# Kernel optimization log

Hardware: AMD Instinct MI355X
Metric: run time of the kernel (lower is better)

Reference implementation:

```python
import jax, jax.numpy as jnp
import numpy as np

# Norse LIFParameters defaults (method='super', alpha=100)
DT = 1e-3
TAU_SYN_INV = 200.0   # 1 / 5e-3
TAU_MEM_INV = 100.0   # 1 / 1e-2
V_TH = 1.0
V_LEAK = 0.0
V_RESET = 0.0
ALPHA = 100.0

@jax.custom_vjp
def superspike(x):
    return (x > 0).astype(x.dtype)

def _ss_fwd(x):
    return superspike(x), x

def _ss_bwd(x, g):
    return (g / (ALPHA * jnp.abs(x) + 1.0) ** 2,)

superspike.defvjp(_ss_fwd, _ss_bwd)

T, B, F, H1, OUT = 100, 512, 784, 1024, 10

def setup_inputs() -> dict:
    key = jax.random.key(0)
    k1, k2, k3 = jax.random.split(key, 3)
    x = jax.random.normal(k1, (T, B, F), jnp.float32)
    # fc0: Linear(784, h1) with bias
    W0 = jax.random.normal(k2, (H1, F), jnp.float32) / np.sqrt(F)
    b0 = jnp.zeros((H1,), jnp.float32)
    # LILinearCell input_weights: Linear(h1, 10) without bias
    Wout = jax.random.normal(k3, (OUT, H1), jnp.float32) / np.sqrt(H1)
    return {"x": x, "W0": W0, "b0": b0, "Wout": Wout}

def reference(x, W0, b0, Wout):
    Tn, Bn, Fn = x.shape
    H = W0.shape[0]
    O = Wout.shape[0]

    def step(state, xt):
        v_lif, i_lif, v_li, i_li = state
        z_in = xt @ W0.T + b0                                    # [B, H]
        # LIF cell step
        v_dec = v_lif + DT * TAU_MEM_INV * ((V_LEAK - v_lif) + i_lif)
        i_dec = i_lif * (1.0 - DT * TAU_SYN_INV)
        z = superspike(v_dec - V_TH)                             # spikes [B, H]
        v_new = (1.0 - z) * v_dec + z * V_RESET
        i_new = i_dec + z_in
        # LI linear cell step (voltage output)
        v_li_new = v_li + DT * TAU_MEM_INV * ((V_LEAK - v_li) + i_li)
        i_li_new = i_li * (1.0 - DT * TAU_SYN_INV) + z @ Wout.T  # [B, O]
        return (v_new, i_new, v_li_new, i_li_new), v_li_new

    z0 = lambda s: jnp.zeros(s, x.dtype)
    init = (z0((Bn, H)), z0((Bn, H)), z0((Bn, O)), z0((Bn, O)))
    _, voltages = jax.lax.scan(step, init, x)
    return voltages  # [T, B, 10]
```

## Files before the change

### kernel.cpp

```cpp
#include <hip/hip_runtime.h>

#define T_TOT 100
#define BATCH 512
#define FIN   784
#define HID   1024
#define NOUT  10
#define KP    800
#define BK    32
#define KSTEPS 25

typedef _Float16 f16x8 __attribute__((ext_vector_type(8)));
typedef float    f32x4 __attribute__((ext_vector_type(4)));

#define AS1C(p) ((const __attribute__((address_space(1))) void*)(p))
#define AS3(p)  ((__attribute__((address_space(3))) void*)(p))

__global__ __launch_bounds__(256)
void cvt_split(const float* __restrict__ src, _Float16* __restrict__ hi,
               _Float16* __restrict__ lo, int nrows)
{
    int idx = blockIdx.x * 256 + threadIdx.x;
    if (idx >= nrows * 100) return;
    int row = idx / 100;
    int k0  = (idx - row * 100) * 8;
    f16x8 h, l;
    if (k0 < FIN) {
        float4 a = *(const float4*)(src + (size_t)row * FIN + k0);
        float4 b = *(const float4*)(src + (size_t)row * FIN + k0 + 4);
        float xs[8] = {a.x, a.y, a.z, a.w, b.x, b.y, b.z, b.w};
        #pragma unroll
        for (int j = 0; j < 8; ++j) {
            _Float16 hh = (_Float16)xs[j];
            h[j] = hh;
            l[j] = (_Float16)((xs[j] - (float)hh) * 4096.0f);
        }
    } else {
        #pragma unroll
        for (int j = 0; j < 8; ++j) { h[j] = (_Float16)0.f; l[j] = (_Float16)0.f; }
    }
    *(f16x8*)(hi + (size_t)row * KP + k0) = h;
    *(f16x8*)(lo + (size_t)row * KP + k0) = l;
}

__global__ __launch_bounds__(256, 2)
void gemm_mfma(const _Float16* __restrict__ Xhi, const _Float16* __restrict__ Xlo,
               const _Float16* __restrict__ Whi, const _Float16* __restrict__ Wlo,
               const float* __restrict__ bias, float* __restrict__ Z, int mb)
{
    __shared__ char smem[65536];
    const int tid  = threadIdx.x;
    const int lane = tid & 63;
    const int wid  = tid >> 6;
    const int wm   = wid >> 1;
    const int wn   = wid & 1;
    const int fr   = lane & 15;
    const int fg   = lane >> 4;

    const int j = blockIdx.x;
    int bm, bn;
    if ((mb & 7) == 0) {
        bm = (j & 7) | ((j >> 6) << 3);
        bn = (j >> 3) & 7;
    } else {
        bm = j >> 3;
        bn = j & 7;
    }
    const size_t row0 = (size_t)bm * 128;
    const int    col0 = bn * 128;

    f32x4 accm[4][4], accc[4][4];
    #pragma unroll
    for (int a = 0; a < 4; ++a)
        #pragma unroll
        for (int b = 0; b < 4; ++b) {
            accm[a][b] = (f32x4){0.f, 0.f, 0.f, 0.f};
            accc[a][b] = (f32x4){0.f, 0.f, 0.f, 0.f};
        }

    auto stage = [&](int buf, int kt) {
        const int kof = kt * BK;
        #pragma unroll
        for (int q = 0; q < 2; ++q) {
            const int lin = q * 256 + tid;
            const int row = lin >> 2;
            const int pos = lin & 3;
            const int gg  = pos ^ ((row >> 1) & 3);
            const int ldsw = buf * 32768 + q * 4096 + wid * 1024;
            const size_t ga = (row0 + row) * (size_t)KP + kof + gg * 8;
            const size_t gb = (size_t)(col0 + row) * KP + kof + gg * 8;
            __builtin_amdgcn_global_load_lds(AS1C(Xhi + ga), AS3(smem + ldsw),         16, 0, 0);
            __builtin_amdgcn_global_load_lds(AS1C(Xlo + ga), AS3(smem + ldsw +  8192), 16, 0, 0);
            __builtin_amdgcn_global_load_lds(AS1C(Whi + gb), AS3(smem + ldsw + 16384), 16, 0, 0);
            __builtin_amdgcn_global_load_lds(AS1C(Wlo + gb), AS3(smem + ldsw + 24576), 16, 0, 0);
        }
    };

    auto compute = [&](int buf) {
        const char* base = smem + buf * 32768;
        f16x8 ah[4], al[4], bh[4], bl[4];
        #pragma unroll
        for (int mf = 0; mf < 4; ++mf) {
            const int row = wm * 64 + mf * 16 + fr;
            const int off = row * 64 + ((fg ^ ((row >> 1) & 3)) << 4);
            ah[mf] = *(const f16x8*)(base + off);
            al[mf] = *(const f16x8*)(base + 8192 + off);
        }
        #pragma unroll
        for (int nf = 0; nf < 4; ++nf) {
            const int row = wn * 64 + nf * 16 + fr;
            const int off = row * 64 + ((fg ^ ((row >> 1) & 3)) << 4);
            bh[nf] = *(const f16x8*)(base + 16384 + off);
            bl[nf] = *(const f16x8*)(base + 24576 + off);
        }
        #pragma unroll
        for (int mf = 0; mf < 4; ++mf)
            #pragma unroll
            for (int nf = 0; nf < 4; ++nf) {
                accm[mf][nf] = __builtin_amdgcn_mfma_f32_16x16x32_f16(ah[mf], bh[nf], accm[mf][nf], 0, 0, 0);
                accc[mf][nf] = __builtin_amdgcn_mfma_f32_16x16x32_f16(ah[mf], bl[nf], accc[mf][nf], 0, 0, 0);
                accc[mf][nf] = __builtin_amdgcn_mfma_f32_16x16x32_f16(al[mf], bh[nf], accc[mf][nf], 0, 0, 0);
            }
    };

    stage(0, 0);
    int buf = 0;
    for (int kt = 0; kt < KSTEPS; ++kt) {
        __syncthreads();
        if (kt + 1 < KSTEPS) stage(buf ^ 1, kt + 1);
        compute(buf);
        buf ^= 1;
    }

    #pragma unroll
    for (int nf = 0; nf < 4; ++nf) {
        const int colg = col0 + wn * 64 + nf * 16 + fr;
        const float bv = bias[colg];
        #pragma unroll
        for (int mf = 0; mf < 4; ++mf) {
            const size_t rowg = row0 + wm * 64 + mf * 16 + fg * 4;
            #pragma unroll
            for (int i = 0; i < 4; ++i)
                Z[(rowg + i) * HID + colg] =
                    accm[mf][nf][i] + accc[mf][nf][i] * 2.44140625e-4f + bv;
        }
    }
}

__global__ __launch_bounds__(256, 2)
void lif_scan(const float* __restrict__ Z, const float* __restrict__ Wout,
              float* __restrict__ out,
              float* __restrict__ st_v, float* __restrict__ st_i,
              float* __restrict__ st_vli, float* __restrict__ st_ili,
              int t0, int tn, int first, int last)
{
#pragma clang fp contract(off)
    __shared__ float Wlds[NOUT][HID];
    __shared__ float red[2][4][NOUT];

    const int tid  = threadIdx.x;
    const int b    = blockIdx.x;
    const int h4   = tid * 4;
    const int lane = tid & 63;
    const int wv   = tid >> 6;

    #pragma unroll
    for (int o = 0; o < NOUT; ++o)
        *(float4*)&Wlds[o][h4] = *(const float4*)&Wout[o * HID + h4];

    float v[4], cu[4];
    if (first) {
        #pragma unroll
        for (int j = 0; j < 4; ++j) { v[j] = 0.f; cu[j] = 0.f; }
    } else {
        float4 tv = *(const float4*)&st_v[(size_t)b*HID + h4];
        float4 ti = *(const float4*)&st_i[(size_t)b*HID + h4];
        v[0]=tv.x; v[1]=tv.y; v[2]=tv.z; v[3]=tv.w;
        cu[0]=ti.x; cu[1]=ti.y; cu[2]=ti.z; cu[3]=ti.w;
    }
    float vli = 0.f, ili = 0.f;
    if (!first && tid < NOUT) {
        vli = st_vli[b*NOUT + tid];
        ili = st_ili[b*NOUT + tid];
    }

    __syncthreads();

    const float* Zb = Z + (size_t)b * HID + h4;
    float4 zn = *(const float4*)Zb;

    for (int t = 0; t < tn; ++t) {
        float4 zc = zn;
        if (t + 1 < tn) zn = *(const float4*)(Zb + (size_t)(t+1) * BATCH * HID);

        const float za[4] = {zc.x, zc.y, zc.z, zc.w};
        float zf[4];
        bool anyz = false;
        #pragma unroll
        for (int j = 0; j < 4; ++j) {
            float tmp  = (0.0f - v[j]) + cu[j];
            float vdec = v[j] + 0.1f * tmp;
            bool  z    = vdec > 1.0f;
            zf[j] = z ? 1.0f : 0.0f;
            anyz  = anyz || z;
            v[j]  = z ? 0.0f : vdec;
            cu[j] = cu[j] * 0.8f + za[j];
        }

        float p[NOUT];
        #pragma unroll
        for (int o = 0; o < NOUT; ++o) p[o] = 0.f;

        if (__any(anyz)) {
            if (anyz) {
                #pragma unroll
                for (int o = 0; o < NOUT; ++o) {
                    float4 w = *(const float4*)&Wlds[o][h4];
                    p[o] = zf[0]*w.x + zf[1]*w.y + zf[2]*w.z + zf[3]*w.w;
                }
            }
            #pragma unroll
            for (int o = 0; o < NOUT; ++o) {
                float s = p[o];
                s += __shfl_xor(s, 1);
                s += __shfl_xor(s, 2);
                s += __shfl_xor(s, 4);
                s += __shfl_xor(s, 8);
                s += __shfl_xor(s, 16);
                s += __shfl_xor(s, 32);
                p[o] = s;
            }
        }

        const int par = t & 1;
        if (lane == 0) {
            #pragma unroll
            for (int o = 0; o < NOUT; ++o) red[par][wv][o] = p[o];
        }
        __syncthreads();
        if (tid < NOUT) {
            float s = red[par][0][tid] + red[par][1][tid]
                    + red[par][2][tid] + red[par][3][tid];
            float tmp  = (0.0f - vli) + ili;
            float vnew = vli + 0.1f * tmp;
            ili = ili * 0.8f + s;
            vli = vnew;
            out[((size_t)(t0 + t) * BATCH + b) * NOUT + tid] = vnew;
        }
    }

    if (!last) {
        *(float4*)&st_v[(size_t)b*HID + h4] = make_float4(v[0], v[1], v[2], v[3]);
        *(float4*)&st_i[(size_t)b*HID + h4] = make_float4(cu[0], cu[1], cu[2], cu[3]);
        if (tid < NOUT) { st_vli[b*NOUT + tid] = vli; st_ili[b*NOUT + tid] = ili; }
    }
}

extern "C" void kernel_launch(void* const* d_in, const int* in_sizes, int n_in,
                              void* d_out, int out_size, void* d_ws, size_t ws_size,
                              hipStream_t stream)
{
    const float* x    = (const float*)d_in[0];
    const float* W0   = (const float*)d_in[1];
    const float* b0   = (const float*)d_in[2];
    const float* Wout = (const float*)d_in[3];
    float* out = (float*)d_out;

    char* ws = (char*)d_ws;
    float* st_v   = (float*)ws;
    float* st_i   = st_v   + (size_t)BATCH * HID;
    float* st_vli = st_i   + (size_t)BATCH * HID;
    float* st_ili = st_vli + BATCH * NOUT;
    _Float16* Whi = (_Float16*)(st_ili + BATCH * NOUT);
    _Float16* Wlo = Whi + (size_t)HID * KP;
    char* dyn = (char*)(Wlo + (size_t)HID * KP);

    const size_t fixed = (size_t)(dyn - ws);
    const size_t per_t = (size_t)BATCH * HID * 4
                       + (size_t)BATCH * KP * 2 * 2;
    size_t avail = (ws_size > fixed) ? ws_size - fixed : 0;
    int tch = (int)(avail / per_t);
    if (tch > T_TOT) tch = T_TOT;
    if (tch >= 2) tch &= ~1;
    if (tch < 1) tch = 1;

    float*    Zbuf = (float*)dyn;
    _Float16* Xhi  = (_Float16*)(dyn + (size_t)tch * BATCH * HID * 4);
    _Float16* Xlo  = Xhi + (size_t)tch * BATCH * KP;

    hipLaunchKernelGGL(cvt_split, dim3((HID * 100 + 255) / 256), dim3(256), 0, stream,
                       W0, Whi, Wlo, HID);

    for (int t0 = 0; t0 < T_TOT; t0 += tch) {
        const int tn    = (T_TOT - t0 < tch) ? (T_TOT - t0) : tch;
        const int nrows = tn * BATCH;
        const int mb    = nrows / 128;

        hipLaunchKernelGGL(cvt_split, dim3((nrows * 100 + 255) / 256), dim3(256), 0, stream,
                           x + (size_t)t0 * BATCH * FIN, Xhi, Xlo, nrows);
        hipLaunchKernelGGL(gemm_mfma, dim3(mb * 8), dim3(256), 0, stream,
                           Xhi, Xlo, Whi, Wlo, b0, Zbuf, mb);
        hipLaunchKernelGGL(lif_scan, dim3(BATCH), dim3(256), 0, stream,
                           Zbuf, Wout, out, st_v, st_i, st_vli, st_ili,
                           t0, tn, (t0 == 0) ? 1 : 0, (t0 + tn >= T_TOT) ? 1 : 0);
    }
}
```

Baseline: 537.4 us.

## Use 8-wave GEMM with triple-buffered LDS pipeline and DPP reductions in scan

The GEMM goes from 4 waves to 8 waves per 128x128 tile, with each wave holding half as many accumulators. Staging moves to a 3-stage LDS ring that waits with vmcnt and a raw s_barrier, and MFMA priority is raised with setprio. The block index mapping is also changed for L2 locality. In the LIF scan, the cross-lane reduction becomes DPP sums within 16-lane groups over 16 partial slots, and Z is prefetched two timesteps ahead. Risks: more LDS per block (96KB), which may limit occupancy, and the vmcnt-only wait across waves relies on the barrier for correctness.

```diff
diff --git a/kernel.cpp b/kernel.cpp
--- a/kernel.cpp
+++ b/kernel.cpp
@@ -8,6 +8,14 @@
 #define KP    800
 #define BK    32
 #define KSTEPS 25
+
+#define BM 128
+#define BN 128
+#define BUFSZ 32768
+#define A_HI 0
+#define A_LO 8192
+#define B_HI 16384
+#define B_LO 24576
 
 typedef _Float16 f16x8 __attribute__((ext_vector_type(8)));
 typedef float    f32x4 __attribute__((ext_vector_type(4)));
@@ -42,12 +50,12 @@
     *(f16x8*)(lo + (size_t)row * KP + k0) = l;
 }
 
-__global__ __launch_bounds__(256, 2)
+__global__ __launch_bounds__(512, 2)
 void gemm_mfma(const _Float16* __restrict__ Xhi, const _Float16* __restrict__ Xlo,
                const _Float16* __restrict__ Whi, const _Float16* __restrict__ Wlo,
                const float* __restrict__ bias, float* __restrict__ Z, int mb)
 {
-    __shared__ char smem[65536];
+    __shared__ char smem[3 * BUFSZ];
     const int tid  = threadIdx.x;
     const int lane = tid & 63;
     const int wid  = tid >> 6;
@@ -59,76 +67,80 @@
     const int j = blockIdx.x;
     int bm, bn;
     if ((mb & 7) == 0) {
-        bm = (j & 7) | ((j >> 6) << 3);
-        bn = (j >> 3) & 7;
+        const int x = j & 7, r = j >> 3;
+        bm = x * (mb >> 3) + (r >> 3);
+        bn = r & 7;
     } else {
         bm = j >> 3;
         bn = j & 7;
     }
-    const size_t row0 = (size_t)bm * 128;
-    const int    col0 = bn * 128;
-
-    f32x4 accm[4][4], accc[4][4];
+    const size_t row0 = (size_t)bm * BM;
+    const int    col0 = bn * BN;
+
+    const int srow = tid >> 2;
+    const int spos = tid & 3;
+    const int sgg  = spos ^ ((srow >> 1) & 3);
+    const size_t gax = (row0 + srow) * (size_t)KP + sgg * 8;
+    const size_t gbx = (size_t)(col0 + srow) * KP + sgg * 8;
+    const int ldsw = wid * 1024;
+
+    auto stage = [&](int buf, int kt) {
+        const int kof = kt * BK;
+        const char* dummy;
+        char* base = smem + buf * BUFSZ + ldsw;
+        __builtin_amdgcn_global_load_lds(AS1C(Xhi + gax + kof), AS3(base + A_HI), 16, 0, 0);
+        __builtin_amdgcn_global_load_lds(AS1C(Xlo + gax + kof), AS3(base + A_LO), 16, 0, 0);
+        __builtin_amdgcn_global_load_lds(AS1C(Whi + gbx + kof), AS3(base + B_HI), 16, 0, 0);
+        __builtin_amdgcn_global_load_lds(AS1C(Wlo + gbx + kof), AS3(base + B_LO), 16, 0, 0);
+        (void)dummy;
+    };
+
+    f32x4 accm[2][4], accc[2][4];
     #pragma unroll
-    for (int a = 0; a < 4; ++a)
+    for (int a = 0; a < 2; ++a)
         #pragma unroll
         for (int b = 0; b < 4; ++b) {
             accm[a][b] = (f32x4){0.f, 0.f, 0.f, 0.f};
             accc[a][b] = (f32x4){0.f, 0.f, 0.f, 0.f};
         }
 
-    auto stage = [&](int buf, int kt) {
-        const int kof = kt * BK;
-        #pragma unroll
-        for (int q = 0; q < 2; ++q) {
-            const int lin = q * 256 + tid;
-            const int row = lin >> 2;
-            const int pos = lin & 3;
-            const int gg  = pos ^ ((row >> 1) & 3);
-            const int ldsw = buf * 32768 + q * 4096 + wid * 1024;
-            const size_t ga = (row0 + row) * (size_t)KP + kof + gg * 8;
-            const size_t gb = (size_t)(col0 + row) * KP + kof + gg * 8;
-            __builtin_amdgcn_global_load_lds(AS1C(Xhi + ga), AS3(smem + ldsw),         16, 0, 0);
-            __builtin_amdgcn_global_load_lds(AS1C(Xlo + ga), AS3(smem + ldsw +  8192), 16, 0, 0);
-            __builtin_amdgcn_global_load_lds(AS1C(Whi + gb), AS3(smem + ldsw + 16384), 16, 0, 0);
-            __builtin_amdgcn_global_load_lds(AS1C(Wlo + gb), AS3(smem + ldsw + 24576), 16, 0, 0);
-        }
-    };
-
     auto compute = [&](int buf) {
-        const char* base = smem + buf * 32768;
-        f16x8 ah[4], al[4], bh[4], bl[4];
-        #pragma unroll
-        for (int mf = 0; mf < 4; ++mf) {
-            const int row = wm * 64 + mf * 16 + fr;
+        const char* base = smem + buf * BUFSZ;
+        f16x8 ah[2], al[2], bh[4], bl[4];
+        #pragma unroll
+        for (int mf = 0; mf < 2; ++mf) {
+            const int row = wm * 32 + mf * 16 + fr;
             const int off = row * 64 + ((fg ^ ((row >> 1) & 3)) << 4);
-            ah[mf] = *(const f16x8*)(base + off);
-            al[mf] = *(const f16x8*)(base + 8192 + off);
+            ah[mf] = *(const f16x8*)(base + A_HI + off);
+            al[mf] = *(const f16x8*)(base + A_LO + off);
         }
         #pragma unroll
         for (int nf = 0; nf < 4; ++nf) {
             const int row = wn * 64 + nf * 16 + fr;
             const int off = row * 64 + ((fg ^ ((row >> 1) & 3)) << 4);
-            bh[nf] = *(const f16x8*)(base + 16384 + off);
-            bl[nf] = *(const f16x8*)(base + 24576 + off);
-        }
-        #pragma unroll
-        for (int mf = 0; mf < 4; ++mf)
+            bh[nf] = *(const f16x8*)(base + B_HI + off);
+            bl[nf] = *(const f16x8*)(base + B_LO + off);
+        }
+        __builtin_amdgcn_s_setprio(1);
+        #pragma unroll
+        for (int mf = 0; mf < 2; ++mf)
             #pragma unroll
             for (int nf = 0; nf < 4; ++nf) {
                 accm[mf][nf] = __builtin_amdgcn_mfma_f32_16x16x32_f16(ah[mf], bh[nf], accm[mf][nf], 0, 0, 0);
                 accc[mf][nf] = __builtin_amdgcn_mfma_f32_16x16x32_f16(ah[mf], bl[nf], accc[mf][nf], 0, 0, 0);
                 accc[mf][nf] = __builtin_amdgcn_mfma_f32_16x16x32_f16(al[mf], bh[nf], accc[mf][nf], 0, 0, 0);
             }
+        __builtin_amdgcn_s_setprio(0);
     };
 
     stage(0, 0);
-    int buf = 0;
+    stage(1, 1);
     for (int kt = 0; kt < KSTEPS; ++kt) {
-        __syncthreads();
-        if (kt + 1 < KSTEPS) stage(buf ^ 1, kt + 1);
-        compute(buf);
-        buf ^= 1;
+        if (kt < KSTEPS - 1) asm volatile("s_waitcnt vmcnt(4)" ::: "memory");
+        else                 asm volatile("s_waitcnt vmcnt(0)" ::: "memory");
+        __builtin_amdgcn_s_barrier();
+        if (kt + 2 < KSTEPS) stage((kt + 2) % 3, kt + 2);
+        compute(kt % 3);
     }
 
     #pragma unroll
@@ -136,14 +148,28 @@
         const int colg = col0 + wn * 64 + nf * 16 + fr;
         const float bv = bias[colg];
         #pragma unroll
-        for (int mf = 0; mf < 4; ++mf) {
-            const size_t rowg = row0 + wm * 64 + mf * 16 + fg * 4;
+        for (int mf = 0; mf < 2; ++mf) {
+            const size_t rowg = row0 + wm * 32 + mf * 16 + fg * 4;
             #pragma unroll
             for (int i = 0; i < 4; ++i)
                 Z[(rowg + i) * HID + colg] =
                     accm[mf][nf][i] + accc[mf][nf][i] * 2.44140625e-4f + bv;
         }
     }
+}
+
+__device__ __forceinline__ float dpp_sum16(float v)
+{
+    int x;
+    x = __builtin_amdgcn_update_dpp(0, __builtin_bit_cast(int, v), 0xB1, 0xF, 0xF, true);
+    v += __builtin_bit_cast(float, x);
+    x = __builtin_amdgcn_update_dpp(0, __builtin_bit_cast(int, v), 0x4E, 0xF, 0xF, true);
+    v += __builtin_bit_cast(float, x);
+    x = __builtin_amdgcn_update_dpp(0, __builtin_bit_cast(int, v), 0x141, 0xF, 0xF, true);
+    v += __builtin_bit_cast(float, x);
+    x = __builtin_amdgcn_update_dpp(0, __builtin_bit_cast(int, v), 0x140, 0xF, 0xF, true);
+    v += __builtin_bit_cast(float, x);
+    return v;
 }
 
 __global__ __launch_bounds__(256, 2)
@@ -155,7 +181,7 @@
 {
 #pragma clang fp contract(off)
     __shared__ float Wlds[NOUT][HID];
-    __shared__ float red[2][4][NOUT];
+    __shared__ float red[2][16][NOUT];
 
     const int tid  = threadIdx.x;
     const int b    = blockIdx.x;
@@ -186,11 +212,14 @@
     __syncthreads();
 
     const float* Zb = Z + (size_t)b * HID + h4;
-    float4 zn = *(const float4*)Zb;
+    float4 zn  = *(const float4*)Zb;
+    float4 znn = (tn > 1) ? *(const float4*)(Zb + (size_t)BATCH * HID)
+                          : zn;
 
     for (int t = 0; t < tn; ++t) {
         float4 zc = zn;
-        if (t + 1 < tn) zn = *(const float4*)(Zb + (size_t)(t+1) * BATCH * HID);
+        zn = znn;
+        if (t + 2 < tn) znn = *(const float4*)(Zb + (size_t)(t+2) * BATCH * HID);
 
         const float za[4] = {zc.x, zc.y, zc.z, zc.w};
         float zf[4];
@@ -219,27 +248,20 @@
                 }
             }
             #pragma unroll
-            for (int o = 0; o < NOUT; ++o) {
-                float s = p[o];
-                s += __shfl_xor(s, 1);
-                s += __shfl_xor(s, 2);
-                s += __shfl_xor(s, 4);
-                s += __shfl_xor(s, 8);
-                s += __shfl_xor(s, 16);
-                s += __shfl_xor(s, 32);
-                p[o] = s;
-            }
+            for (int o = 0; o < NOUT; ++o) p[o] = dpp_sum16(p[o]);
         }
 
         const int par = t & 1;
-        if (lane == 0) {
-            #pragma unroll
-            for (int o = 0; o < NOUT; ++o) red[par][wv][o] = p[o];
+        if ((lane & 15) == 0) {
+            const int g = wv * 4 + (lane >> 4);
+            #pragma unroll
+            for (int o = 0; o < NOUT; ++o) red[par][g][o] = p[o];
         }
         __syncthreads();
         if (tid < NOUT) {
-            float s = red[par][0][tid] + red[par][1][tid]
-                    + red[par][2][tid] + red[par][3][tid];
+            float s = 0.f;
+            #pragma unroll
+            for (int g = 0; g < 16; ++g) s += red[par][g][tid];
             float tmp  = (0.0f - vli) + ili;
             float vnew = vli + 0.1f * tmp;
             ili = ili * 0.8f + s;
@@ -280,7 +302,7 @@
     size_t avail = (ws_size > fixed) ? ws_size - fixed : 0;
     int tch = (int)(avail / per_t);
     if (tch > T_TOT) tch = T_TOT;
-    if (tch >= 2) tch &= ~1;
+    if (tch >= 4) tch &= ~3;
     if (tch < 1) tch = 1;
 
     float*    Zbuf = (float*)dyn;
@@ -293,11 +315,11 @@
     for (int t0 = 0; t0 < T_TOT; t0 += tch) {
         const int tn    = (T_TOT - t0 < tch) ? (T_TOT - t0) : tch;
         const int nrows = tn * BATCH;
-        const int mb    = nrows / 128;
+        const int mb    = nrows / BM;
 
         hipLaunchKernelGGL(cvt_split, dim3((nrows * 100 + 255) / 256), dim3(256), 0, stream,
                            x + (size_t)t0 * BATCH * FIN, Xhi, Xlo, nrows);
-        hipLaunchKernelGGL(gemm_mfma, dim3(mb * 8), dim3(256), 0, stream,
+        hipLaunchKernelGGL(gemm_mfma, dim3(mb * 8), dim3(512), 0, stream,
                            Xhi, Xlo, Whi, Wlo, b0, Zbuf, mb);
         hipLaunchKernelGGL(lif_scan, dim3(BATCH), dim3(256), 0, stream,
                            Zbuf, Wout, out, st_v, st_i, st_vli, st_ili,
```

After: 539.6 us. Within noise of the previous version (+0.4%).
